# Kernel tuning notes

Hardware: AMD Instinct MI355X
Metric: run time of the kernel (lower is better)

Reference implementation:

```python
import jax, jax.numpy as jnp
import numpy as np

B, T, D = 4, 4096, 1024
EPS = 1e-5  # FusedRMSNormSwishGate default eps


def setup_inputs() -> dict:
    key = jax.random.key(0)
    ks = jax.random.split(key, 6)
    s = 1.0 / np.sqrt(D)
    return {
        "x": jax.random.normal(ks[0], (B, T, D), jnp.float32),
        "Wi": jax.random.normal(ks[1], (D, D), jnp.float32) * s,
        "Wf": jax.random.normal(ks[2], (D, D), jnp.float32) * s,
        "Wg": jax.random.normal(ks[3], (D, D), jnp.float32) * s,
        "Wo": jax.random.normal(ks[4], (D, D), jnp.float32) * s,
        "norm_w": jnp.ones((D,), jnp.float32),
    }


def _hgrn_scan(f, i):
    # h_t = f_t * h_{t-1} + i_t  (elementwise gated linear recurrence)
    # associative combine: (f1,i1) o (f2,i2) = (f1*f2, i1*f2 + i2)
    def combine(a, b):
        fa, ia = a
        fb, ib = b
        return fa * fb, ia * fb + ib

    _, h = jax.lax.associative_scan(combine, (f, i), axis=1)
    return h


def reference(x, Wi, Wf, Wg, Wo, norm_w):
    # projections
    i = x @ Wi.T                                  # [B,T,D]
    f = jax.nn.sigmoid(x @ Wf.T)                  # forget gate in (0,1)
    # swiglu(i, 1-f): silu on the value, gated by the input gate (1-f)
    inp = jax.nn.silu(i) * (1.0 - f)
    # hierarchically-gated linear recurrence (chunk/parallel scan form)
    h = _hgrn_scan(f, inp)                        # [B,T,D]
    # RMSNorm(h) * swish(g) output gate
    g = x @ Wg.T
    rms = h * jax.lax.rsqrt(jnp.mean(h * h, axis=-1, keepdims=True) + EPS)
    o = (rms * norm_w) * (g * jax.nn.sigmoid(g))
    return o @ Wo.T
```

## Files before the change

kernel.cpp:

```cpp
#include <hip/hip_runtime.h>
#include <hip/hip_bf16.h>

typedef unsigned short u16;
using bf16x8 = __bf16 __attribute__((ext_vector_type(8)));
using f32x4  = float  __attribute__((ext_vector_type(4)));

#define BB 4
#define TT 4096
#define DD 1024
#define MROWS (BB*TT)
#define CT 64
#define NC (TT/CT)

__device__ __forceinline__ float sigm(float x) { return 1.0f / (1.0f + __expf(-x)); }
__device__ __forceinline__ u16 f2bf(float f) {
    __hip_bfloat16 h = __float2bfloat16(f);
    return *reinterpret_cast<u16*>(&h);
}
__device__ __forceinline__ float bf2f(u16 u) { return __uint_as_float(((unsigned)u) << 16); }

__device__ __forceinline__ void async_cp16(const u16* g, u16* l) {
    __builtin_amdgcn_global_load_lds(
        (const __attribute__((address_space(1))) unsigned int*)g,
        (__attribute__((address_space(3))) unsigned int*)l, 16, 0, 0);
}

__global__ __launch_bounds__(256) void conv_x_kernel(const float* __restrict__ s,
                                                     u16* __restrict__ d) {
    size_t i = (size_t)blockIdx.x * 256 + threadIdx.x;
    float4 v = *(const float4*)(s + i * 4);
    ushort4 u;
    u.x = f2bf(v.x); u.y = f2bf(v.y); u.z = f2bf(v.z); u.w = f2bf(v.w);
    *(ushort4*)(d + i * 4) = u;
}

__global__ __launch_bounds__(256) void conv_w4_kernel(const float* __restrict__ w0,
                                                      const float* __restrict__ w1,
                                                      const float* __restrict__ w2,
                                                      const float* __restrict__ w3,
                                                      u16* __restrict__ dst) {
    int i = blockIdx.x * 256 + threadIdx.x;
    int sel = i >> 18;
    int off = i & 262143;
    const float* s = (sel == 0) ? w0 : (sel == 1) ? w1 : (sel == 2) ? w2 : w3;
    float4 v = *(const float4*)(s + (size_t)off * 4);
    ushort4 u;
    u.x = f2bf(v.x); u.y = f2bf(v.y); u.z = f2bf(v.z); u.w = f2bf(v.w);
    *(ushort4*)(dst + ((size_t)sel << 20) + (size_t)off * 4) = u;
}

#define BM 128
#define BN 128
#define BK 64

template <typename OutT>
__global__ __launch_bounds__(256, 2)
void gemm_bf16_bt(const u16* __restrict__ Ag, const u16* __restrict__ Bg, int K,
                  OutT* __restrict__ P0, OutT* __restrict__ P1, OutT* __restrict__ P2) {
    __shared__ u16 As[BM * BK];
    __shared__ u16 Bs[BN * BK];

    const int tid  = threadIdx.x;
    const int lane = tid & 63;
    const int wid  = tid >> 6;
    const int wm   = wid >> 1;
    const int wn   = wid & 1;
    const int lr   = lane & 15;
    const int lq   = lane >> 4;

    const int nwg  = gridDim.x * gridDim.y;
    const int flat = blockIdx.y * gridDim.x + blockIdx.x;
    const int cpx  = nwg >> 3;
    const int swz  = (flat & 7) * cpx + (flat >> 3);
    const int bx   = swz % gridDim.x;
    const int by   = swz / gridDim.x;

    const long bM  = (long)by * BM;
    const long bN0 = (long)bx * BN;

    const f32x4 zero = {0.f, 0.f, 0.f, 0.f};
    f32x4 acc[4][4];
#pragma unroll
    for (int i = 0; i < 4; i++)
#pragma unroll
        for (int j = 0; j < 4; j++) acc[i][j] = zero;

    for (int kt = 0; kt < K; kt += BK) {
        __syncthreads();
#pragma unroll
        for (int j = 0; j < 4; j++) {
            const int G  = j * 256 + tid;
            const int m  = G >> 3;
            const int p  = G & 7;
            const int gk = p ^ (m & 7);
            async_cp16(Ag + (bM + m) * K + kt + gk * 8, &As[G * 8]);
            async_cp16(Bg + (bN0 + m) * K + kt + gk * 8, &Bs[G * 8]);
        }
        __syncthreads();
#pragma unroll
        for (int kk = 0; kk < BK / 32; kk++) {
            bf16x8 av[4], bv[4];
#pragma unroll
            for (int f = 0; f < 4; f++) {
                const int am = wm * 64 + f * 16 + lr;
                const int ag = (kk * 4 + lq) ^ (am & 7);
                av[f] = *(const bf16x8*)(&As[am * 64 + ag * 8]);
                const int bn = wn * 64 + f * 16 + lr;
                const int bg = (kk * 4 + lq) ^ (bn & 7);
                bv[f] = *(const bf16x8*)(&Bs[bn * 64 + bg * 8]);
            }
#pragma unroll
            for (int i = 0; i < 4; i++)
#pragma unroll
                for (int j = 0; j < 4; j++)
                    acc[i][j] = __builtin_amdgcn_mfma_f32_16x16x32_bf16(av[i], bv[j],
                                                                        acc[i][j], 0, 0, 0);
        }
    }

    const int pl = (int)(bN0 >> 10);
    OutT* P = (pl == 0) ? P0 : ((pl == 1) ? P1 : P2);
    const int cn = (int)(bN0 & 1023);
#pragma unroll
    for (int i = 0; i < 4; i++) {
        const long m0 = bM + wm * 64 + i * 16 + lq * 4;
#pragma unroll
        for (int j = 0; j < 4; j++) {
            const int n = cn + wn * 64 + j * 16 + lr;
#pragma unroll
            for (int r = 0; r < 4; r++) {
                if constexpr (sizeof(OutT) == 2)
                    P[(m0 + r) * 1024 + n] = f2bf(acc[i][j][r]);
                else
                    P[(m0 + r) * 1024 + n] = acc[i][j][r];
            }
        }
    }
}

__global__ __launch_bounds__(256) void scan_pass1(const u16* __restrict__ ip,
                                                  const u16* __restrict__ fp,
                                                  float* __restrict__ Fc,
                                                  float* __restrict__ Ic) {
    const int tid = blockIdx.x * 256 + threadIdx.x;
    const int d4  = tid & 255;
    const int c   = (tid >> 8) & (NC - 1);
    const int b   = tid >> 14;
    size_t base = ((size_t)(b * TT + c * CT) << 10) + (size_t)d4 * 4;
    float F[4] = {1.f, 1.f, 1.f, 1.f};
    float I[4] = {0.f, 0.f, 0.f, 0.f};
#pragma unroll 8
    for (int t = 0; t < CT; t++) {
        ushort4 fu = *(const ushort4*)(fp + base);
        ushort4 iu = *(const ushort4*)(ip + base);
        base += DD;
        const u16 fa[4] = {fu.x, fu.y, fu.z, fu.w};
        const u16 ia[4] = {iu.x, iu.y, iu.z, iu.w};
#pragma unroll
        for (int j = 0; j < 4; j++) {
            float f  = sigm(bf2f(fa[j]));
            float iv = bf2f(ia[j]);
            float v  = iv * sigm(iv) * (1.f - f);
            I[j] = fmaf(f, I[j], v);
            F[j] *= f;
        }
    }
    const size_t o = (((size_t)(b * NC + c)) << 10) + (size_t)d4 * 4;
    float4 vF = {F[0], F[1], F[2], F[3]};
    float4 vI = {I[0], I[1], I[2], I[3]};
    *(float4*)(Fc + o) = vF;
    *(float4*)(Ic + o) = vI;
}

__global__ __launch_bounds__(256) void scan_pass2(const float* __restrict__ Fc,
                                                  const float* __restrict__ Ic,
                                                  float* __restrict__ Hin) {
    const int gtid = blockIdx.x * 256 + threadIdx.x;
    const int lane = gtid & 63;
    const int w    = gtid >> 6;
    const int b    = w >> 10;
    const int d    = w & 1023;
    const int idx  = ((b * NC + lane) << 10) + d;
    float F = Fc[idx];
    float I = Ic[idx];
#pragma unroll
    for (int s = 1; s < 64; s <<= 1) {
        float Fp = __shfl_up(F, s, 64);
        float Ip = __shfl_up(I, s, 64);
        if (lane >= s) {
            I = fmaf(Ip, F, I);
            F *= Fp;
        }
    }
    float Hex = __shfl_up(I, 1, 64);
    if (lane == 0) Hex = 0.f;
    Hin[idx] = Hex;
}

__global__ __launch_bounds__(256) void scan_pass3_norm(const u16* __restrict__ ip,
                                                       const u16* __restrict__ fp,
                                                       const float* __restrict__ Hin,
                                                       const u16* __restrict__ gp,
                                                       const float* __restrict__ w,
                                                       u16* __restrict__ oout) {
    const int t_ = threadIdx.x;
    const int c  = blockIdx.x & (NC - 1);
    const int b  = blockIdx.x >> 6;
    size_t base = ((size_t)(b * TT + c * CT) << 10) + (size_t)t_ * 4;
    const size_t o = (((size_t)(b * NC + c)) << 10) + (size_t)t_ * 4;
    float4 hv = *(const float4*)(Hin + o);
    float h[4] = {hv.x, hv.y, hv.z, hv.w};
    const float4 wv = *(const float4*)(w + (size_t)t_ * 4);
    const float wl[4] = {wv.x, wv.y, wv.z, wv.w};
    __shared__ float red[2][4];
    for (int t = 0; t < CT; t++) {
        ushort4 fu = *(const ushort4*)(fp + base);
        ushort4 iu = *(const ushort4*)(ip + base);
        ushort4 gu = *(const ushort4*)(gp + base);
        const u16 fa[4] = {fu.x, fu.y, fu.z, fu.w};
        const u16 ia[4] = {iu.x, iu.y, iu.z, iu.w};
        const u16 ga[4] = {gu.x, gu.y, gu.z, gu.w};
        float ss = 0.f;
#pragma unroll
        for (int j = 0; j < 4; j++) {
            float f  = sigm(bf2f(fa[j]));
            float iv = bf2f(ia[j]);
            float v  = iv * sigm(iv) * (1.f - f);
            h[j] = fmaf(f, h[j], v);
            ss = fmaf(h[j], h[j], ss);
        }
#pragma unroll
        for (int off = 32; off > 0; off >>= 1) ss += __shfl_down(ss, off);
        if ((t_ & 63) == 0) red[t & 1][t_ >> 6] = ss;
        __syncthreads();
        const float tot = red[t & 1][0] + red[t & 1][1] + red[t & 1][2] + red[t & 1][3];
        const float rms = rsqrtf(tot * (1.f / 1024.f) + 1e-5f);
        ushort4 ou;
        u16 oa[4];
#pragma unroll
        for (int j = 0; j < 4; j++) {
            float gv = bf2f(ga[j]);
            oa[j] = f2bf(h[j] * rms * wl[j] * gv * sigm(gv));
        }
        ou.x = oa[0]; ou.y = oa[1]; ou.z = oa[2]; ou.w = oa[3];
        *(ushort4*)(oout + base) = ou;
        base += DD;
    }
}

extern "C" void kernel_launch(void* const* d_in, const int* in_sizes, int n_in,
                              void* d_out, int out_size, void* d_ws, size_t ws_size,
                              hipStream_t stream) {
    const float* x  = (const float*)d_in[0];
    const float* Wi = (const float*)d_in[1];
    const float* Wf = (const float*)d_in[2];
    const float* Wg = (const float*)d_in[3];
    const float* Wo = (const float*)d_in[4];
    const float* nw = (const float*)d_in[5];
    float* out = (float*)d_out;

    const size_t MB = 1ull << 20;
    char* ws = (char*)d_ws;
    u16*   xo  = (u16*)(ws);
    u16*   Wb  = (u16*)(ws + 32 * MB);
    u16*   Pi  = (u16*)(ws + 40 * MB);
    u16*   Pf  = (u16*)(ws + 72 * MB);
    float* Fc  = (float*)(ws + 104 * MB);
    float* Ic  = Fc + BB * NC * DD;
    float* Hin = Ic + BB * NC * DD;
    u16*   g   = (u16*)d_out;

    conv_x_kernel<<<16384, 256, 0, stream>>>(x, xo);
    conv_w4_kernel<<<4096, 256, 0, stream>>>(Wi, Wf, Wg, Wo, Wb);
    gemm_bf16_bt<u16><<<dim3(24, 128), 256, 0, stream>>>(xo, Wb, 1024, Pi, Pf, g);
    scan_pass1<<<256, 256, 0, stream>>>(Pi, Pf, Fc, Ic);
    scan_pass2<<<1024, 256, 0, stream>>>(Fc, Ic, Hin);
    scan_pass3_norm<<<256, 256, 0, stream>>>(Pi, Pf, Hin, g, nw, xo);
    gemm_bf16_bt<float><<<dim3(8, 128), 256, 0, stream>>>(xo, Wb + 3ull * 1024 * 1024, 1024,
                                                          out, out, out);
}
```

Baseline: 414.9 us.

## Fuse x conversion into GEMM load, split scan3 norm into two phases

Drops the separate fp32-to-bf16 conversion kernel for x. The first GEMM now loads fp32 x into registers, converts it, and writes bf16 into LDS. The final scan kernel now runs the recurrence for the whole chunk first, storing h in a 128KB LDS buffer and per-wave partial sums. This removes the per-timestep __syncthreads. Normalization and gating then happen in a second loop. The GEMM tile swizzle is also removed. The trade-offs are that the A operand is no longer loaded asynchronously, the large LDS footprint limits scan occupancy, and h is rounded to bf16 before normalization.

```diff
diff --git a/kernel.cpp b/kernel.cpp
--- a/kernel.cpp
+++ b/kernel.cpp
@@ -3,6 +3,7 @@
 
 typedef unsigned short u16;
 using bf16x8 = __bf16 __attribute__((ext_vector_type(8)));
+using u16x8  = unsigned short __attribute__((ext_vector_type(8)));
 using f32x4  = float  __attribute__((ext_vector_type(4)));
 
 #define BB 4
@@ -23,15 +24,6 @@
     __builtin_amdgcn_global_load_lds(
         (const __attribute__((address_space(1))) unsigned int*)g,
         (__attribute__((address_space(3))) unsigned int*)l, 16, 0, 0);
-}
-
-__global__ __launch_bounds__(256) void conv_x_kernel(const float* __restrict__ s,
-                                                     u16* __restrict__ d) {
-    size_t i = (size_t)blockIdx.x * 256 + threadIdx.x;
-    float4 v = *(const float4*)(s + i * 4);
-    ushort4 u;
-    u.x = f2bf(v.x); u.y = f2bf(v.y); u.z = f2bf(v.z); u.w = f2bf(v.w);
-    *(ushort4*)(d + i * 4) = u;
 }
 
 __global__ __launch_bounds__(256) void conv_w4_kernel(const float* __restrict__ w0,
@@ -53,10 +45,10 @@
 #define BN 128
 #define BK 64
 
-template <typename OutT>
+template <typename AT, typename OutT>
 __global__ __launch_bounds__(256, 2)
-void gemm_bf16_bt(const u16* __restrict__ Ag, const u16* __restrict__ Bg, int K,
-                  OutT* __restrict__ P0, OutT* __restrict__ P1, OutT* __restrict__ P2) {
+void gemm_bt(const AT* __restrict__ Ag, const u16* __restrict__ Bg, int K,
+             OutT* __restrict__ P0, OutT* __restrict__ P1, OutT* __restrict__ P2) {
     __shared__ u16 As[BM * BK];
     __shared__ u16 Bs[BN * BK];
 
@@ -68,15 +60,8 @@
     const int lr   = lane & 15;
     const int lq   = lane >> 4;
 
-    const int nwg  = gridDim.x * gridDim.y;
-    const int flat = blockIdx.y * gridDim.x + blockIdx.x;
-    const int cpx  = nwg >> 3;
-    const int swz  = (flat & 7) * cpx + (flat >> 3);
-    const int bx   = swz % gridDim.x;
-    const int by   = swz / gridDim.x;
-
-    const long bM  = (long)by * BM;
-    const long bN0 = (long)bx * BN;
+    const long bM  = (long)blockIdx.y * BM;
+    const long bN0 = (long)blockIdx.x * BN;
 
     const f32x4 zero = {0.f, 0.f, 0.f, 0.f};
     f32x4 acc[4][4];
@@ -86,14 +71,34 @@
         for (int j = 0; j < 4; j++) acc[i][j] = zero;
 
     for (int kt = 0; kt < K; kt += BK) {
+        float4 afr[4][2];
+        if constexpr (sizeof(AT) == 4) {
+#pragma unroll
+            for (int j = 0; j < 4; j++) {
+                const int G  = j * 256 + tid;
+                const int m  = G >> 3;
+                const int gk = (G & 7) ^ (m & 7);
+                const float* s = (const float*)Ag + (bM + m) * (long)K + kt + gk * 8;
+                afr[j][0] = *(const float4*)s;
+                afr[j][1] = *(const float4*)(s + 4);
+            }
+        }
         __syncthreads();
 #pragma unroll
         for (int j = 0; j < 4; j++) {
             const int G  = j * 256 + tid;
             const int m  = G >> 3;
-            const int p  = G & 7;
-            const int gk = p ^ (m & 7);
-            async_cp16(Ag + (bM + m) * K + kt + gk * 8, &As[G * 8]);
+            const int gk = (G & 7) ^ (m & 7);
+            if constexpr (sizeof(AT) == 4) {
+                u16x8 wv;
+                wv[0] = f2bf(afr[j][0].x); wv[1] = f2bf(afr[j][0].y);
+                wv[2] = f2bf(afr[j][0].z); wv[3] = f2bf(afr[j][0].w);
+                wv[4] = f2bf(afr[j][1].x); wv[5] = f2bf(afr[j][1].y);
+                wv[6] = f2bf(afr[j][1].z); wv[7] = f2bf(afr[j][1].w);
+                *(u16x8*)(&As[G * 8]) = wv;
+            } else {
+                async_cp16((const u16*)Ag + (bM + m) * (long)K + kt + gk * 8, &As[G * 8]);
+            }
             async_cp16(Bg + (bN0 + m) * K + kt + gk * 8, &Bs[G * 8]);
         }
         __syncthreads();
@@ -197,30 +202,34 @@
     Hin[idx] = Hex;
 }
 
-__global__ __launch_bounds__(256) void scan_pass3_norm(const u16* __restrict__ ip,
-                                                       const u16* __restrict__ fp,
-                                                       const float* __restrict__ Hin,
-                                                       const u16* __restrict__ gp,
-                                                       const float* __restrict__ w,
-                                                       u16* __restrict__ oout) {
-    const int t_ = threadIdx.x;
-    const int c  = blockIdx.x & (NC - 1);
-    const int b  = blockIdx.x >> 6;
+__global__ __launch_bounds__(256) void scan3_norm(const u16* __restrict__ ip,
+                                                  const u16* __restrict__ fp,
+                                                  const float* __restrict__ Hin,
+                                                  const u16* __restrict__ gp,
+                                                  const float* __restrict__ w,
+                                                  u16* __restrict__ oout) {
+    __shared__ u16 hlds[CT * DD];
+    __shared__ float sw[4][CT];
+    const int t_   = threadIdx.x;
+    const int lane = t_ & 63;
+    const int wv_  = t_ >> 6;
+    const int c    = blockIdx.x & (NC - 1);
+    const int b    = blockIdx.x >> 6;
     size_t base = ((size_t)(b * TT + c * CT) << 10) + (size_t)t_ * 4;
     const size_t o = (((size_t)(b * NC + c)) << 10) + (size_t)t_ * 4;
     float4 hv = *(const float4*)(Hin + o);
     float h[4] = {hv.x, hv.y, hv.z, hv.w};
-    const float4 wv = *(const float4*)(w + (size_t)t_ * 4);
-    const float wl[4] = {wv.x, wv.y, wv.z, wv.w};
-    __shared__ float red[2][4];
+    size_t rb = base;
+#pragma unroll 4
     for (int t = 0; t < CT; t++) {
-        ushort4 fu = *(const ushort4*)(fp + base);
-        ushort4 iu = *(const ushort4*)(ip + base);
-        ushort4 gu = *(const ushort4*)(gp + base);
+        ushort4 fu = *(const ushort4*)(fp + rb);
+        ushort4 iu = *(const ushort4*)(ip + rb);
+        rb += DD;
         const u16 fa[4] = {fu.x, fu.y, fu.z, fu.w};
         const u16 ia[4] = {iu.x, iu.y, iu.z, iu.w};
-        const u16 ga[4] = {gu.x, gu.y, gu.z, gu.w};
         float ss = 0.f;
+        ushort4 hu;
+        u16 ha[4];
 #pragma unroll
         for (int j = 0; j < 4; j++) {
             float f  = sigm(bf2f(fa[j]));
@@ -228,23 +237,36 @@
             float v  = iv * sigm(iv) * (1.f - f);
             h[j] = fmaf(f, h[j], v);
             ss = fmaf(h[j], h[j], ss);
-        }
+            ha[j] = f2bf(h[j]);
+        }
+        hu.x = ha[0]; hu.y = ha[1]; hu.z = ha[2]; hu.w = ha[3];
+        *(ushort4*)(&hlds[t * DD + t_ * 4]) = hu;
 #pragma unroll
         for (int off = 32; off > 0; off >>= 1) ss += __shfl_down(ss, off);
-        if ((t_ & 63) == 0) red[t & 1][t_ >> 6] = ss;
-        __syncthreads();
-        const float tot = red[t & 1][0] + red[t & 1][1] + red[t & 1][2] + red[t & 1][3];
+        if (lane == 0) sw[wv_][t] = ss;
+    }
+    __syncthreads();
+    const float4 wvv = *(const float4*)(w + (size_t)t_ * 4);
+    const float wl[4] = {wvv.x, wvv.y, wvv.z, wvv.w};
+    size_t wb = base;
+#pragma unroll 4
+    for (int t = 0; t < CT; t++) {
+        const float tot = sw[0][t] + sw[1][t] + sw[2][t] + sw[3][t];
         const float rms = rsqrtf(tot * (1.f / 1024.f) + 1e-5f);
+        ushort4 hu = *(const ushort4*)(&hlds[t * DD + t_ * 4]);
+        ushort4 gu = *(const ushort4*)(gp + wb);
+        const u16 ha[4] = {hu.x, hu.y, hu.z, hu.w};
+        const u16 ga[4] = {gu.x, gu.y, gu.z, gu.w};
         ushort4 ou;
         u16 oa[4];
 #pragma unroll
         for (int j = 0; j < 4; j++) {
             float gv = bf2f(ga[j]);
-            oa[j] = f2bf(h[j] * rms * wl[j] * gv * sigm(gv));
+            oa[j] = f2bf(bf2f(ha[j]) * rms * wl[j] * gv * sigm(gv));
         }
         ou.x = oa[0]; ou.y = oa[1]; ou.z = oa[2]; ou.w = oa[3];
-        *(ushort4*)(oout + base) = ou;
-        base += DD;
+        *(ushort4*)(oout + wb) = ou;
+        wb += DD;
     }
 }
 
@@ -261,7 +283,7 @@
 
     const size_t MB = 1ull << 20;
     char* ws = (char*)d_ws;
-    u16*   xo  = (u16*)(ws);
+    u16*   ob  = (u16*)(ws);
     u16*   Wb  = (u16*)(ws + 32 * MB);
     u16*   Pi  = (u16*)(ws + 40 * MB);
     u16*   Pf  = (u16*)(ws + 72 * MB);
@@ -270,12 +292,11 @@
     float* Hin = Ic + BB * NC * DD;
     u16*   g   = (u16*)d_out;
 
-    conv_x_kernel<<<16384, 256, 0, stream>>>(x, xo);
     conv_w4_kernel<<<4096, 256, 0, stream>>>(Wi, Wf, Wg, Wo, Wb);
-    gemm_bf16_bt<u16><<<dim3(24, 128), 256, 0, stream>>>(xo, Wb, 1024, Pi, Pf, g);
+    gemm_bt<float, u16><<<dim3(24, 128), 256, 0, stream>>>(x, Wb, 1024, Pi, Pf, g);
     scan_pass1<<<256, 256, 0, stream>>>(Pi, Pf, Fc, Ic);
     scan_pass2<<<1024, 256, 0, stream>>>(Fc, Ic, Hin);
-    scan_pass3_norm<<<256, 256, 0, stream>>>(Pi, Pf, Hin, g, nw, xo);
-    gemm_bf16_bt<float><<<dim3(8, 128), 256, 0, stream>>>(xo, Wb + 3ull * 1024 * 1024, 1024,
+    scan3_norm<<<256, 256, 0, stream>>>(Pi, Pf, Hin, g, nw, ob);
+    gemm_bt<u16, float><<<dim3(8, 128), 256, 0, stream>>>(ob, Wb + 3ull * 1024 * 1024, 1024,
                                                           out, out, out);
 }
```

After: 415.9 us. No clear change (+0.2%).
